# Kernel optimization log

Hardware: AMD Instinct MI355X
Metric: run time of the kernel (lower is better)

## Reference

```python
import jax, jax.numpy as jnp
import numpy as np

B, CIN, L = 4, 128, 2048
D_MODEL, D_STATE, EXPAND, HEADDIM, NGROUPS = 256, 16, 3, 3, 1
D_INNER = EXPAND * D_MODEL            # 768
NHEADS = D_INNER // HEADDIM           # 256
CONV_DIM = D_INNER + 2 * NGROUPS * D_STATE   # 800
D_IN_PROJ = 2 * D_INNER + 2 * NGROUPS * D_STATE + NHEADS  # 1824
K_PROJ, D_CONV = 4, 4
EPS = 1e-5


def setup_inputs() -> dict:
    key = jax.random.key(0)
    ks = jax.random.split(key, 9)
    x = jax.random.normal(ks[0], (B, CIN, L), jnp.float32)
    proj_w = jax.random.normal(ks[1], (D_MODEL, CIN, K_PROJ), jnp.float32) / np.float32(np.sqrt(CIN * K_PROJ))
    in_proj_w = jax.random.normal(ks[2], (D_IN_PROJ, D_MODEL), jnp.float32) / np.float32(np.sqrt(D_MODEL))
    conv_w = jax.random.normal(ks[3], (CONV_DIM, 1, D_CONV), jnp.float32) / np.float32(np.sqrt(D_CONV))
    conv_b = jax.random.normal(ks[4], (CONV_DIM,), jnp.float32) * 0.01
    # dt_bias = inverse-softplus of dt ~ LogUniform[1e-3, 1e-1] (mamba2 init)
    u = jax.random.uniform(ks[5], (NHEADS,), jnp.float32)
    dt = jnp.exp(u * np.float32(np.log(0.1) - np.log(1e-3)) + np.float32(np.log(1e-3)))
    dt_bias = dt + jnp.log(-jnp.expm1(-dt))
    A_log = jnp.log(1.0 + 15.0 * jax.random.uniform(ks[6], (NHEADS,), jnp.float32))  # A in [-16,-1]
    D_skip = jnp.ones((NHEADS,), jnp.float32)
    norm_w = jnp.ones((D_INNER,), jnp.float32)
    out_proj_w = jax.random.normal(ks[7], (D_MODEL, D_INNER), jnp.float32) / np.float32(np.sqrt(D_INNER))
    return {"x": x, "proj_w": proj_w, "in_proj_w": in_proj_w, "conv_w": conv_w,
            "conv_b": conv_b, "dt_bias": dt_bias, "A_log": A_log, "D_skip": D_skip,
            "norm_w": norm_w, "out_proj_w": out_proj_w}


def _forward(x, proj_w, in_proj_w, conv_w, conv_b, dt_bias, A_log, D_skip, norm_w, out_proj_w):
    # outer Conv1d, padding='same' (k=4 -> left 1, right 2), no bias: (B,CIN,L)->(B,D_MODEL,L)
    h = jax.lax.conv_general_dilated(x, proj_w, (1,), [(1, 2)],
                                     dimension_numbers=("NCH", "OIH", "NCH"))
    u = h.transpose(0, 2, 1)                          # (B, L, d_model)
    zxbcdt = jnp.einsum("bld,ed->ble", u, in_proj_w)  # (B, L, 1824)
    z = zxbcdt[..., :D_INNER]                                     # (B,L,768)
    xBC = zxbcdt[..., D_INNER:D_INNER + CONV_DIM]                 # (B,L,800)
    dt = zxbcdt[..., D_INNER + CONV_DIM:]                         # (B,L,256)
    dt = jax.nn.softplus(dt + dt_bias)
    # depthwise causal conv (pad d_conv-1 on left) + SiLU
    xBC_c = jax.lax.conv_general_dilated(xBC.transpose(0, 2, 1), conv_w, (1,), [(D_CONV - 1, 0)],
                                         feature_group_count=CONV_DIM,
                                         dimension_numbers=("NCH", "OIH", "NCH"))
    xBC = jax.nn.silu(xBC_c + conv_b[None, :, None]).transpose(0, 2, 1)  # (B,L,800)
    xs = xBC[..., :D_INNER].reshape(B, L, NHEADS, HEADDIM)        # (B,L,H,P)
    Bm = xBC[..., D_INNER:D_INNER + D_STATE]                      # (B,L,N) (ngroups=1)
    Cm = xBC[..., D_INNER + D_STATE:]                             # (B,L,N)
    A = -jnp.exp(A_log)                                           # (H,)

    def step(hst, inp):
        dt_t, x_t, B_t, C_t = inp                 # (B,H),(B,H,P),(B,N),(B,N)
        dA = jnp.exp(dt_t * A)[:, :, None, None]  # (B,H,1,1)
        hst = dA * hst + jnp.einsum("bh,bhp,bn->bhpn", dt_t, x_t, B_t)
        y_t = jnp.einsum("bhpn,bn->bhp", hst, C_t)
        return hst, y_t

    h0 = jnp.zeros((B, NHEADS, HEADDIM, D_STATE), x.dtype)
    _, ys = jax.lax.scan(step, h0, (dt.transpose(1, 0, 2), xs.transpose(1, 0, 2, 3),
                                    Bm.transpose(1, 0, 2), Cm.transpose(1, 0, 2)))
    y = ys.transpose(1, 0, 2, 3) + D_skip[None, None, :, None] * xs   # (B,L,H,P)
    y = y.reshape(B, L, D_INNER)
    # gated RMSNorm: gate first, then normalize (norm_before_gate=False)
    y = y * jax.nn.silu(z)
    y = y * jax.lax.rsqrt(jnp.mean(y * y, axis=-1, keepdims=True) + EPS) * norm_w
    out = jnp.einsum("ble,de->bld", y, out_proj_w)   # (B,L,d_model)
    return out.transpose(0, 2, 1)                    # (B,d_model,L)


def reference(x, proj_w, in_proj_w, conv_w, conv_b, dt_bias, A_log, D_skip, norm_w, out_proj_w):
    return _forward(x, proj_w, in_proj_w, conv_w, conv_b, dt_bias, A_log, D_skip, norm_w, out_proj_w)
```

## Files before the change

### kernel.cpp

```cpp
#include <hip/hip_runtime.h>
#include <hip/hip_fp16.h>
#include <math.h>

#define B_     4
#define CIN    128
#define LEN    2048
#define DMODEL 256
#define DSTATE 16
#define NHEADS 256
#define DINNER 768
#define CONVDIM 800
#define DINPROJ 1824
#define EPS_   1e-5f
#define CHUNK  64
#define NCHUNK 32

typedef _Float16 f16x8 __attribute__((ext_vector_type(8)));
typedef float    f32x4 __attribute__((ext_vector_type(4)));

__device__ __forceinline__ float silu_(float x){ return x / (1.0f + __expf(-x)); }
__device__ __forceinline__ float softplus_(float x){
    return x > 0.f ? x + log1pf(__expf(-x)) : log1pf(__expf(x));
}

__device__ __forceinline__ void gl2lds16(const _Float16* g, _Float16* l){
    __builtin_amdgcn_global_load_lds(
        (const __attribute__((address_space(1))) void*)g,
        (__attribute__((address_space(3))) void*)l, 16, 0, 0);
}

__global__ __launch_bounds__(256) void k_f2h3(const float* __restrict__ a0,
                                              const float* __restrict__ a1,
                                              const float* __restrict__ a2,
                                              _Float16* __restrict__ o0,
                                              _Float16* __restrict__ o1,
                                              _Float16* __restrict__ o2,
                                              int n0, int n1, int n2){
    int total = n0 + n1 + n2;
    for (int i = blockIdx.x * 256 + threadIdx.x; i < total; i += gridDim.x * 256){
        if (i < n0)            o0[i] = (_Float16)a0[i];
        else if (i < n0 + n1)  o1[i - n0] = (_Float16)a1[i - n0];
        else                   o2[i - n0 - n1] = (_Float16)a2[i - n0 - n1];
    }
}

__global__ __launch_bounds__(256) void k_im2col(const float* __restrict__ x,
                                                _Float16* __restrict__ xcol){
    __shared__ float xs[CIN][68];
    int blk = blockIdx.x;
    int b  = blk >> 5;
    int l0 = (blk & 31) << 6;
    const float* xb = x + (size_t)b * CIN * LEN;
    for (int idx = threadIdx.x; idx < CIN * 67; idx += 256){
        int ci = idx / 67, j = idx % 67;
        int gl = l0 - 1 + j;
        xs[ci][j] = (gl >= 0 && gl < LEN) ? xb[ci * LEN + gl] : 0.f;
    }
    __syncthreads();
    #pragma unroll
    for (int v = 0; v < 16; v++){
        int id = v * 256 + threadIdx.x;
        int rl = id >> 6, c = id & 63;
        f16x8 pk;
        #pragma unroll
        for (int e = 0; e < 8; e++){
            int ci = c * 2 + (e >> 2), k = e & 3;
            pk[e] = (_Float16)xs[ci][rl + k];
        }
        *(f16x8*)&xcol[((size_t)(b * LEN + l0 + rl)) * 512 + c * 8] = pk;
    }
}

template<int K, int EPI>
__global__ __launch_bounds__(256) void k_gemm(const _Float16* __restrict__ A,
                                              const _Float16* __restrict__ Bw,
                                              const float* __restrict__ dt_bias,
                                              _Float16* __restrict__ o_u,
                                              _Float16* __restrict__ o_z,
                                              _Float16* __restrict__ o_xbc,
                                              _Float16* __restrict__ o_dt,
                                              float* __restrict__ o_f){
    __shared__ __align__(16) _Float16 As[128 * 32];
    __shared__ __align__(16) _Float16 Bs[128 * 32];
    int tid  = threadIdx.x;
    int wv   = tid >> 6;
    int lane = tid & 63;
    int quad = lane >> 4;
    int l16  = lane & 15;
    int m0 = blockIdx.x * 128;
    int n0 = blockIdx.y * 128;
    int wm = (wv >> 1) * 64;
    int wn = (wv & 1) * 64;
    int srow = lane >> 2;
    int scol = (lane & 3) * 8;

    f32x4 acc[4][4];
    #pragma unroll
    for (int i = 0; i < 4; i++)
        #pragma unroll
        for (int j = 0; j < 4; j++)
            acc[i][j] = (f32x4){0.f, 0.f, 0.f, 0.f};

    for (int k0 = 0; k0 < K; k0 += 32){
        #pragma unroll
        for (int j = 0; j < 2; j++){
            int ar = m0 + wv * 32 + j * 16 + srow;
            gl2lds16(A + (size_t)ar * K + k0 + scol,
                     &As[(wv * 32 + j * 16) * 32]);
            int nr = n0 + wv * 32 + j * 16 + srow;
            if (EPI == 1) nr = nr > (DINPROJ - 1) ? (DINPROJ - 1) : nr;
            gl2lds16(Bw + (size_t)nr * K + k0 + scol,
                     &Bs[(wv * 32 + j * 16) * 32]);
        }
        __syncthreads();
        f16x8 af[4], bf[4];
        #pragma unroll
        for (int i = 0; i < 4; i++)
            af[i] = *(const f16x8*)&As[(wm + i * 16 + l16) * 32 + quad * 8];
        #pragma unroll
        for (int j = 0; j < 4; j++)
            bf[j] = *(const f16x8*)&Bs[(wn + j * 16 + l16) * 32 + quad * 8];
        #pragma unroll
        for (int i = 0; i < 4; i++)
            #pragma unroll
            for (int j = 0; j < 4; j++)
                acc[i][j] = __builtin_amdgcn_mfma_f32_16x16x32_f16(
                                af[i], bf[j], acc[i][j], 0, 0, 0);
        __syncthreads();
    }

    if (EPI == 0){
        #pragma unroll
        for (int j = 0; j < 4; j++){
            int col = n0 + wn + j * 16 + l16;
            #pragma unroll
            for (int i = 0; i < 4; i++){
                int row = m0 + wm + i * 16 + quad * 4;
                #pragma unroll
                for (int r = 0; r < 4; r++)
                    o_u[(size_t)(row + r) * DMODEL + col] = (_Float16)acc[i][j][r];
            }
        }
    } else if (EPI == 1){
        #pragma unroll
        for (int j = 0; j < 4; j++){
            int col = n0 + wn + j * 16 + l16;
            if (col < DINNER){
                #pragma unroll
                for (int i = 0; i < 4; i++){
                    int row = m0 + wm + i * 16 + quad * 4;
                    #pragma unroll
                    for (int r = 0; r < 4; r++)
                        o_z[(size_t)(row + r) * DINNER + col] = (_Float16)acc[i][j][r];
                }
            } else if (col < DINNER + CONVDIM){
                int cc = col - DINNER;
                #pragma unroll
                for (int i = 0; i < 4; i++){
                    int row = m0 + wm + i * 16 + quad * 4;
                    #pragma unroll
                    for (int r = 0; r < 4; r++)
                        o_xbc[(size_t)(row + r) * CONVDIM + cc] = (_Float16)acc[i][j][r];
                }
            } else if (col < DINPROJ){
                int hh = col - (DINNER + CONVDIM);
                float bias = dt_bias[hh];
                #pragma unroll
                for (int i = 0; i < 4; i++){
                    int row = m0 + wm + i * 16 + quad * 4;
                    #pragma unroll
                    for (int r = 0; r < 4; r++)
                        o_dt[(size_t)(row + r) * NHEADS + hh] =
                            (_Float16)softplus_(acc[i][j][r] + bias);
                }
            }
        }
    } else {
        #pragma unroll
        for (int i = 0; i < 4; i++){
            int row = m0 + wm + i * 16 + quad * 4;
            int b = row >> 11, l = row & (LEN - 1);
            #pragma unroll
            for (int j = 0; j < 4; j++){
                int d = n0 + wn + j * 16 + l16;
                *(f32x4*)&o_f[(((size_t)(b * DMODEL + d)) << 11) + l] = acc[i][j];
            }
        }
    }
}

__global__ __launch_bounds__(256) void k_dwconv(const __half* __restrict__ xbc,
                                                const float* __restrict__ cw,
                                                const float* __restrict__ cb,
                                                __half* __restrict__ xcc){
    int idx = blockIdx.x * 256 + threadIdx.x;
    int seg = idx % 100;
    int r   = idx / 100;
    int l   = r & (LEN - 1);
    int c8  = seg * 8;
    const _Float16* base = (const _Float16*)xbc + (size_t)r * CONVDIM + c8;
    f16x8 zv = {0, 0, 0, 0, 0, 0, 0, 0};
    f16x8 x3 = *(const f16x8*)base;
    f16x8 x2 = (l >= 1) ? *(const f16x8*)(base - CONVDIM) : zv;
    f16x8 x1 = (l >= 2) ? *(const f16x8*)(base - 2 * CONVDIM) : zv;
    f16x8 x0 = (l >= 3) ? *(const f16x8*)(base - 3 * CONVDIM) : zv;
    f16x8 o;
    #pragma unroll
    for (int e = 0; e < 8; e++){
        float4 wv = *(const float4*)(cw + (size_t)(c8 + e) * 4);
        float acc = cb[c8 + e]
                  + (float)x0[e] * wv.x + (float)x1[e] * wv.y
                  + (float)x2[e] * wv.z + (float)x3[e] * wv.w;
        o[e] = (_Float16)silu_(acc);
    }
    *(f16x8*)((_Float16*)xcc + (size_t)r * CONVDIM + c8) = o;
}

__global__ __launch_bounds__(256) void k_scanAC(const __half* __restrict__ dtb,
                                                const __half* __restrict__ xcc,
                                                const float* __restrict__ A_log,
                                                const float* __restrict__ D_skip,
                                                __half* __restrict__ y,
                                                __half* __restrict__ cstate,
                                                float* __restrict__ dsum){
    int wave = threadIdx.x >> 6;
    int task = blockIdx.x * 4 + wave;
    int c  = task & (NCHUNK - 1);
    int hg = (task >> 5) & 63;
    int b  = task >> 11;
    int lane = threadIdx.x & 63;
    int hl = lane >> 4;
    int n  = lane & 15;
    int h  = hg * 4 + hl;
    int c0 = h * 3;
    float A   = -__expf(A_log[h]);
    float Dsk = D_skip[h];
    int t0 = c * CHUNK;
    const __half* xr  = xcc + ((size_t)b * LEN + t0) * CONVDIM;
    const __half* dtp = dtb + ((size_t)b * LEN + t0) * NHEADS + h;
    float h0 = 0.f, h1 = 0.f, h2 = 0.f, sdt = 0.f;
    __half* yp = y + ((size_t)b * LEN + t0) * DINNER + c0;
    for (int t = 0; t < CHUNK; t++){
        float vx0 = __half2float(xr[c0]);
        float vx1 = __half2float(xr[c0 + 1]);
        float vx2 = __half2float(xr[c0 + 2]);
        float vB  = __half2float(xr[DINNER + n]);
        float vC  = __half2float(xr[DINNER + DSTATE + n]);
        float cdt = __half2float(dtp[(size_t)t * NHEADS]);
        float dA  = __expf(cdt * A);
        float dtB = cdt * vB;
        h0 = fmaf(h0, dA, vx0 * dtB);
        h1 = fmaf(h1, dA, vx1 * dtB);
        h2 = fmaf(h2, dA, vx2 * dtB);
        sdt += cdt;
        float p0 = h0 * vC, p1 = h1 * vC, p2 = h2 * vC;
        #pragma unroll
        for (int m = 1; m < 16; m <<= 1){
            p0 += __shfl_xor(p0, m, 64);
            p1 += __shfl_xor(p1, m, 64);
            p2 += __shfl_xor(p2, m, 64);
        }
        if (n < 3){
            float pv = (n == 0) ? p0 : ((n == 1) ? p1 : p2);
            float xv = (n == 0) ? vx0 : ((n == 1) ? vx1 : vx2);
            yp[n] = __float2half(fmaf(Dsk, xv, pv));
        }
        xr += CONVDIM;
        yp += DINNER;
    }
    size_t sbase = (((size_t)(b * NHEADS + h)) * NCHUNK + c) * 48;
    cstate[sbase + n]      = __float2half(h0);
    cstate[sbase + 16 + n] = __float2half(h1);
    cstate[sbase + 32 + n] = __float2half(h2);
    if (n == 0) dsum[(size_t)(b * NHEADS + h) * NCHUNK + c] = __expf(A * sdt);
}

__global__ __launch_bounds__(64) void k_scanB(__half* __restrict__ cstate,
                                              const float* __restrict__ dsum){
    int bh = blockIdx.x;
    int lane = threadIdx.x;
    if (lane >= 48) return;
    __half* st = cstate + (size_t)bh * NCHUNK * 48 + lane;
    const float* dd = dsum + (size_t)bh * NCHUNK;
    float H = 0.f;
    for (int c = 0; c < NCHUNK; c++){
        float d = dd[c];
        float s = __half2float(st[(size_t)c * 48]);
        st[(size_t)c * 48] = __float2half(H);
        H = fmaf(H, d, s);
    }
}

__global__ __launch_bounds__(256) void k_fixup(const __half* __restrict__ dtb,
                                               const __half* __restrict__ xcc,
                                               const float* __restrict__ A_log,
                                               const __half* __restrict__ cstate,
                                               __half* __restrict__ y){
    __shared__ __align__(16) _Float16 decay[32][256];
    __shared__ __align__(16) _Float16 Cs[32][16];
    int blk = blockIdx.x;
    int th = blk & 1;
    int c  = (blk >> 1) & 31;
    int b  = blk >> 6;
    int tid = threadIdx.x;
    int base_t = th * 32;
    size_t row0 = (size_t)b * LEN + c * CHUNK;

    if (tid < 64){
        int i = tid >> 1, k = tid & 1;
        *(f16x8*)&Cs[i][k * 8] =
            *(const f16x8*)((const _Float16*)xcc +
                            (row0 + base_t + i) * CONVDIM + DINNER + DSTATE + k * 8);
    }
    {
        float A = -__expf(A_log[tid]);
        float cum = 0.f;
        const _Float16* dp = (const _Float16*)dtb + row0 * NHEADS + tid;
        for (int t = 0; t < CHUNK; t++){
            cum += (float)dp[(size_t)t * NHEADS];
            if (t >= base_t && t < base_t + 32)
                decay[t - base_t][tid] = (_Float16)__expf(A * cum);
        }
    }
    __syncthreads();

    const _Float16* hp = (const _Float16*)cstate +
                         (((size_t)(b * NHEADS + tid)) * NCHUNK + c) * 48;
    float Hi[3][16];
    #pragma unroll
    for (int p = 0; p < 3; p++){
        f16x8 a = *(const f16x8*)(hp + p * 16);
        f16x8 bq = *(const f16x8*)(hp + p * 16 + 8);
        #pragma unroll
        for (int e = 0; e < 8; e++){ Hi[p][e] = (float)a[e]; Hi[p][8 + e] = (float)bq[e]; }
    }
    __half* yb = y + (row0 + base_t) * DINNER + tid * 3;
    for (int i = 0; i < 32; i++){
        float s0 = 0.f, s1 = 0.f, s2 = 0.f;
        #pragma unroll
        for (int nn = 0; nn < 16; nn++){
            float cv = (float)Cs[i][nn];
            s0 = fmaf(cv, Hi[0][nn], s0);
            s1 = fmaf(cv, Hi[1][nn], s1);
            s2 = fmaf(cv, Hi[2][nn], s2);
        }
        float d = (float)decay[i][tid];
        __half* yp = yb + (size_t)i * DINNER;
        yp[0] = __float2half(__half2float(yp[0]) + d * s0);
        yp[1] = __float2half(__half2float(yp[1]) + d * s1);
        yp[2] = __float2half(__half2float(yp[2]) + d * s2);
    }
}

__global__ __launch_bounds__(256) void k_norm(__half* __restrict__ y,
                                              const __half* __restrict__ z,
                                              const float* __restrict__ nw){
    __shared__ float wsum[4];
    size_t r = blockIdx.x;
    int tid = threadIdx.x;
    const __half* zr = z + r * DINNER;
    __half* yr = y + r * DINNER;
    int e0 = tid, e1 = tid + 256, e2 = tid + 512;
    float t0 = __half2float(yr[e0]) * silu_(__half2float(zr[e0]));
    float t1 = __half2float(yr[e1]) * silu_(__half2float(zr[e1]));
    float t2 = __half2float(yr[e2]) * silu_(__half2float(zr[e2]));
    float ss = t0 * t0 + t1 * t1 + t2 * t2;
    #pragma unroll
    for (int m = 1; m < 64; m <<= 1) ss += __shfl_xor(ss, m, 64);
    if ((tid & 63) == 0) wsum[tid >> 6] = ss;
    __syncthreads();
    float tot = wsum[0] + wsum[1] + wsum[2] + wsum[3];
    float sc = rsqrtf(tot / (float)DINNER + EPS_);
    yr[e0] = __float2half(t0 * sc * nw[e0]);
    yr[e1] = __float2half(t1 * sc * nw[e1]);
    yr[e2] = __float2half(t2 * sc * nw[e2]);
}

extern "C" void kernel_launch(void* const* d_in, const int* in_sizes, int n_in,
                              void* d_out, int out_size, void* d_ws, size_t ws_size,
                              hipStream_t stream) {
    const float* x          = (const float*)d_in[0];
    const float* proj_w     = (const float*)d_in[1];
    const float* in_proj_w  = (const float*)d_in[2];
    const float* conv_w     = (const float*)d_in[3];
    const float* conv_b     = (const float*)d_in[4];
    const float* dt_bias    = (const float*)d_in[5];
    const float* A_log      = (const float*)d_in[6];
    const float* D_skip     = (const float*)d_in[7];
    const float* norm_w     = (const float*)d_in[8];
    const float* out_proj_w = (const float*)d_in[9];
    float* out = (float*)d_out;

    char* ob = (char*)d_out;
    _Float16* pw_h  = (_Float16*)ob;
    _Float16* ipw_h = (_Float16*)(ob + 262144);

    char* wsb = (char*)d_ws;
    _Float16* xcol  = (_Float16*)(wsb);
    _Float16* u_h   = (_Float16*)(wsb + 8388608);
    __half*   xcc_h = (__half*)(wsb);
    __half*   z_h   = (__half*)(wsb + 13107200);
    __half*   xbc_h = (__half*)(wsb + 25690112);
    __half*   y_h   = xbc_h;
    __half*   dt_h  = (__half*)(wsb + 38797312);
    __half*   cstate= (__half*)(wsb + 42991616);
    float*    dsum  = (float*)(wsb + 46137344);
    _Float16* opw_h = (_Float16*)(wsb + 46268416);

    k_f2h3  <<<96, 256, 0, stream>>>(proj_w, in_proj_w, out_proj_w,
                                     pw_h, ipw_h, opw_h,
                                     DMODEL * CIN * 4, DINPROJ * DMODEL,
                                     DMODEL * DINNER);
    k_im2col<<<128, 256, 0, stream>>>(x, xcol);
    k_gemm<512, 0><<<dim3(64, 2), 256, 0, stream>>>(xcol, pw_h, nullptr,
        u_h, nullptr, nullptr, nullptr, nullptr);
    k_gemm<256, 1><<<dim3(64, 15), 256, 0, stream>>>(u_h, ipw_h, dt_bias,
        nullptr, (_Float16*)z_h, (_Float16*)xbc_h, (_Float16*)dt_h, nullptr);
    k_dwconv<<<3200, 256, 0, stream>>>(xbc_h, conv_w, conv_b, xcc_h);
    k_scanAC<<<2048, 256, 0, stream>>>(dt_h, xcc_h, A_log, D_skip, y_h, cstate, dsum);
    k_scanB <<<1024, 64, 0, stream>>>(cstate, dsum);
    k_fixup <<<256, 256, 0, stream>>>(dt_h, xcc_h, A_log, cstate, y_h);
    k_norm  <<<8192, 256, 0, stream>>>(y_h, z_h, norm_w);
    k_gemm<768, 2><<<dim3(64, 2), 256, 0, stream>>>((const _Float16*)y_h, opw_h,
        nullptr, nullptr, nullptr, nullptr, nullptr, out);
}
```

Measured before the change: 320.3 us.

## Merge prep kernels, stage GEMM epilogue through LDS, prefetch scan inputs

Merges the weight fp16 conversion and the im2col kernels into a single launch, with blocks split by index, which removes one kernel launch. The fp16-output GEMM epilogues now write the tile into padded LDS and store 16-byte vectors per row instead of scattered 2-byte stores, and apply softplus per vector for the dt columns. The chunked scan loads the next timestep's inputs before computing the current one, to hide memory latency. LDS use grows to about 34 KB for two of the GEMM variants, which may reduce occupancy.

New measurement: 372.3 us. 16.2% more time.

```diff
diff --git a/kernel.cpp b/kernel.cpp
--- a/kernel.cpp
+++ b/kernel.cpp
@@ -29,45 +29,46 @@
         (__attribute__((address_space(3))) void*)l, 16, 0, 0);
 }
 
-__global__ __launch_bounds__(256) void k_f2h3(const float* __restrict__ a0,
+__global__ __launch_bounds__(256) void k_prep(const float* __restrict__ x,
+                                              const float* __restrict__ a0,
                                               const float* __restrict__ a1,
                                               const float* __restrict__ a2,
                                               _Float16* __restrict__ o0,
                                               _Float16* __restrict__ o1,
                                               _Float16* __restrict__ o2,
-                                              int n0, int n1, int n2){
-    int total = n0 + n1 + n2;
-    for (int i = blockIdx.x * 256 + threadIdx.x; i < total; i += gridDim.x * 256){
-        if (i < n0)            o0[i] = (_Float16)a0[i];
-        else if (i < n0 + n1)  o1[i - n0] = (_Float16)a1[i - n0];
-        else                   o2[i - n0 - n1] = (_Float16)a2[i - n0 - n1];
-    }
-}
-
-__global__ __launch_bounds__(256) void k_im2col(const float* __restrict__ x,
-                                                _Float16* __restrict__ xcol){
+                                              _Float16* __restrict__ xcol){
     __shared__ float xs[CIN][68];
-    int blk = blockIdx.x;
-    int b  = blk >> 5;
-    int l0 = (blk & 31) << 6;
-    const float* xb = x + (size_t)b * CIN * LEN;
-    for (int idx = threadIdx.x; idx < CIN * 67; idx += 256){
-        int ci = idx / 67, j = idx % 67;
-        int gl = l0 - 1 + j;
-        xs[ci][j] = (gl >= 0 && gl < LEN) ? xb[ci * LEN + gl] : 0.f;
-    }
-    __syncthreads();
-    #pragma unroll
-    for (int v = 0; v < 16; v++){
-        int id = v * 256 + threadIdx.x;
-        int rl = id >> 6, c = id & 63;
-        f16x8 pk;
-        #pragma unroll
-        for (int e = 0; e < 8; e++){
-            int ci = c * 2 + (e >> 2), k = e & 3;
-            pk[e] = (_Float16)xs[ci][rl + k];
-        }
-        *(f16x8*)&xcol[((size_t)(b * LEN + l0 + rl)) * 512 + c * 8] = pk;
+    if (blockIdx.x < 128){
+        int blk = blockIdx.x;
+        int b  = blk >> 5;
+        int l0 = (blk & 31) << 6;
+        const float* xb = x + (size_t)b * CIN * LEN;
+        for (int idx = threadIdx.x; idx < CIN * 67; idx += 256){
+            int ci = idx / 67, j = idx % 67;
+            int gl = l0 - 1 + j;
+            xs[ci][j] = (gl >= 0 && gl < LEN) ? xb[ci * LEN + gl] : 0.f;
+        }
+        __syncthreads();
+        #pragma unroll
+        for (int v = 0; v < 16; v++){
+            int id = v * 256 + threadIdx.x;
+            int rl = id >> 6, c = id & 63;
+            f16x8 pk;
+            #pragma unroll
+            for (int e = 0; e < 8; e++){
+                int ci = c * 2 + (e >> 2), k = e & 3;
+                pk[e] = (_Float16)xs[ci][rl + k];
+            }
+            *(f16x8*)&xcol[((size_t)(b * LEN + l0 + rl)) * 512 + c * 8] = pk;
+        }
+    } else {
+        const int n0 = DMODEL * CIN * 4, n1 = DINPROJ * DMODEL, n2 = DMODEL * DINNER;
+        int total = n0 + n1 + n2;
+        for (int i = (blockIdx.x - 128) * 256 + threadIdx.x; i < total; i += 96 * 256){
+            if (i < n0)            o0[i] = (_Float16)a0[i];
+            else if (i < n0 + n1)  o1[i - n0] = (_Float16)a1[i - n0];
+            else                   o2[i - n0 - n1] = (_Float16)a2[i - n0 - n1];
+        }
     }
 }
 
@@ -80,8 +81,10 @@
                                               _Float16* __restrict__ o_xbc,
                                               _Float16* __restrict__ o_dt,
                                               float* __restrict__ o_f){
-    __shared__ __align__(16) _Float16 As[128 * 32];
-    __shared__ __align__(16) _Float16 Bs[128 * 32];
+    __shared__ __align__(16) char smem[(EPI == 2) ? 16384 : 34816];
+    _Float16* As = (_Float16*)smem;
+    _Float16* Bs = (_Float16*)(smem + 8192);
+    _Float16* Ct = (_Float16*)smem;
     int tid  = threadIdx.x;
     int wv   = tid >> 6;
     int lane = tid & 63;
@@ -129,53 +132,7 @@
         __syncthreads();
     }
 
-    if (EPI == 0){
-        #pragma unroll
-        for (int j = 0; j < 4; j++){
-            int col = n0 + wn + j * 16 + l16;
-            #pragma unroll
-            for (int i = 0; i < 4; i++){
-                int row = m0 + wm + i * 16 + quad * 4;
-                #pragma unroll
-                for (int r = 0; r < 4; r++)
-                    o_u[(size_t)(row + r) * DMODEL + col] = (_Float16)acc[i][j][r];
-            }
-        }
-    } else if (EPI == 1){
-        #pragma unroll
-        for (int j = 0; j < 4; j++){
-            int col = n0 + wn + j * 16 + l16;
-            if (col < DINNER){
-                #pragma unroll
-                for (int i = 0; i < 4; i++){
-                    int row = m0 + wm + i * 16 + quad * 4;
-                    #pragma unroll
-                    for (int r = 0; r < 4; r++)
-                        o_z[(size_t)(row + r) * DINNER + col] = (_Float16)acc[i][j][r];
-                }
-            } else if (col < DINNER + CONVDIM){
-                int cc = col - DINNER;
-                #pragma unroll
-                for (int i = 0; i < 4; i++){
-                    int row = m0 + wm + i * 16 + quad * 4;
-                    #pragma unroll
-                    for (int r = 0; r < 4; r++)
-                        o_xbc[(size_t)(row + r) * CONVDIM + cc] = (_Float16)acc[i][j][r];
-                }
-            } else if (col < DINPROJ){
-                int hh = col - (DINNER + CONVDIM);
-                float bias = dt_bias[hh];
-                #pragma unroll
-                for (int i = 0; i < 4; i++){
-                    int row = m0 + wm + i * 16 + quad * 4;
-                    #pragma unroll
-                    for (int r = 0; r < 4; r++)
-                        o_dt[(size_t)(row + r) * NHEADS + hh] =
-                            (_Float16)softplus_(acc[i][j][r] + bias);
-                }
-            }
-        }
-    } else {
+    if (EPI == 2){
         #pragma unroll
         for (int i = 0; i < 4; i++){
             int row = m0 + wm + i * 16 + quad * 4;
@@ -184,6 +141,40 @@
             for (int j = 0; j < 4; j++){
                 int d = n0 + wn + j * 16 + l16;
                 *(f32x4*)&o_f[(((size_t)(b * DMODEL + d)) << 11) + l] = acc[i][j];
+            }
+        }
+    } else {
+        #pragma unroll
+        for (int i = 0; i < 4; i++)
+            #pragma unroll
+            for (int j = 0; j < 4; j++)
+                #pragma unroll
+                for (int r = 0; r < 4; r++)
+                    Ct[(wm + i * 16 + quad * 4 + r) * 136 + wn + j * 16 + l16] =
+                        (_Float16)acc[i][j][r];
+        __syncthreads();
+        #pragma unroll
+        for (int k = 0; k < 8; k++){
+            int cid = tid + k * 256;
+            int row = cid >> 4, ck = cid & 15;
+            int grow = m0 + row;
+            int col = n0 + ck * 8;
+            f16x8 v = *(const f16x8*)&Ct[row * 136 + ck * 8];
+            if (EPI == 0){
+                *(f16x8*)&o_u[(size_t)grow * DMODEL + col] = v;
+            } else {
+                if (col < DINNER){
+                    *(f16x8*)&o_z[(size_t)grow * DINNER + col] = v;
+                } else if (col < DINNER + CONVDIM){
+                    *(f16x8*)&o_xbc[(size_t)grow * CONVDIM + (col - DINNER)] = v;
+                } else if (col < DINPROJ){
+                    int hh = col - (DINNER + CONVDIM);
+                    f16x8 o;
+                    #pragma unroll
+                    for (int e = 0; e < 8; e++)
+                        o[e] = (_Float16)softplus_((float)v[e] + dt_bias[hh + e]);
+                    *(f16x8*)&o_dt[(size_t)grow * NHEADS + hh] = o;
+                }
             }
         }
     }
@@ -236,17 +227,26 @@
     float A   = -__expf(A_log[h]);
     float Dsk = D_skip[h];
     int t0 = c * CHUNK;
-    const __half* xr  = xcc + ((size_t)b * LEN + t0) * CONVDIM;
-    const __half* dtp = dtb + ((size_t)b * LEN + t0) * NHEADS + h;
+    const __half* xrow = xcc + ((size_t)b * LEN + t0) * CONVDIM;
+    const __half* dtp  = dtb + ((size_t)b * LEN + t0) * NHEADS + h;
     float h0 = 0.f, h1 = 0.f, h2 = 0.f, sdt = 0.f;
     __half* yp = y + ((size_t)b * LEN + t0) * DINNER + c0;
+    float vx0 = __half2float(xrow[c0]);
+    float vx1 = __half2float(xrow[c0 + 1]);
+    float vx2 = __half2float(xrow[c0 + 2]);
+    float vB  = __half2float(xrow[DINNER + n]);
+    float vC  = __half2float(xrow[DINNER + DSTATE + n]);
+    float cdt = __half2float(dtp[0]);
     for (int t = 0; t < CHUNK; t++){
-        float vx0 = __half2float(xr[c0]);
-        float vx1 = __half2float(xr[c0 + 1]);
-        float vx2 = __half2float(xr[c0 + 2]);
-        float vB  = __half2float(xr[DINNER + n]);
-        float vC  = __half2float(xr[DINNER + DSTATE + n]);
-        float cdt = __half2float(dtp[(size_t)t * NHEADS]);
+        int tn = (t + 1 < CHUNK) ? t + 1 : t;
+        const __half* xr = xrow + (size_t)tn * CONVDIM;
+        float nx0 = __half2float(xr[c0]);
+        float nx1 = __half2float(xr[c0 + 1]);
+        float nx2 = __half2float(xr[c0 + 2]);
+        float nB  = __half2float(xr[DINNER + n]);
+        float nC  = __half2float(xr[DINNER + DSTATE + n]);
+        float ndt = __half2float(dtp[(size_t)tn * NHEADS]);
+
         float dA  = __expf(cdt * A);
         float dtB = cdt * vB;
         h0 = fmaf(h0, dA, vx0 * dtB);
@@ -265,8 +265,8 @@
             float xv = (n == 0) ? vx0 : ((n == 1) ? vx1 : vx2);
             yp[n] = __float2half(fmaf(Dsk, xv, pv));
         }
-        xr += CONVDIM;
         yp += DINNER;
+        vx0 = nx0; vx1 = nx1; vx2 = nx2; vB = nB; vC = nC; cdt = ndt;
     }
     size_t sbase = (((size_t)(b * NHEADS + h)) * NCHUNK + c) * 48;
     cstate[sbase + n]      = __float2half(h0);
@@ -407,11 +407,8 @@
     float*    dsum  = (float*)(wsb + 46137344);
     _Float16* opw_h = (_Float16*)(wsb + 46268416);
 
-    k_f2h3  <<<96, 256, 0, stream>>>(proj_w, in_proj_w, out_proj_w,
-                                     pw_h, ipw_h, opw_h,
-                                     DMODEL * CIN * 4, DINPROJ * DMODEL,
-                                     DMODEL * DINNER);
-    k_im2col<<<128, 256, 0, stream>>>(x, xcol);
+    k_prep  <<<224, 256, 0, stream>>>(x, proj_w, in_proj_w, out_proj_w,
+                                      pw_h, ipw_h, opw_h, xcol);
     k_gemm<512, 0><<<dim3(64, 2), 256, 0, stream>>>(xcol, pw_h, nullptr,
         u_h, nullptr, nullptr, nullptr, nullptr);
     k_gemm<256, 1><<<dim3(64, 15), 256, 0, stream>>>(u_h, ipw_h, dt_bias,
```
